# Kernel tuning notes

Hardware: AMD Instinct MI355X
Metric: run time of the kernel (lower is better)

## Reference

```python
import jax, jax.numpy as jnp
import numpy as np

N_NODES = 50000


def gcn_conv(x, edge_index, W, b):
    """PyG GCNConv: h = x @ W; add self-loops; symmetric deg^-1/2 norm; scatter-add; + bias."""
    h = x @ W                                   # [N, C_out]
    n = x.shape[0]
    loops = jnp.arange(n, dtype=edge_index.dtype)
    src = jnp.concatenate([edge_index[0], loops])   # [E + N]
    dst = jnp.concatenate([edge_index[1], loops])   # [E + N]
    deg = jax.ops.segment_sum(jnp.ones_like(src, dtype=h.dtype), dst, num_segments=n)
    dinv = jnp.where(deg > 0, jax.lax.rsqrt(deg), 0.0)
    norm = dinv[src] * dinv[dst]                # [E + N]
    msg = h[src] * norm[:, None]                # gather + edgewise scale
    out = jax.ops.segment_sum(msg, dst, num_segments=n)  # scatter-add
    return out + b


def setup_inputs() -> dict:
    key = jax.random.key(0)
    k1, k2, k3, k4 = jax.random.split(key, 4)
    x = jax.random.normal(k1, (N_NODES, 128), dtype=jnp.float32)
    edge_index = jax.random.randint(k2, (2, 800000), 0, N_NODES, dtype=jnp.int32)
    W1 = jax.random.normal(k3, (128, 128), dtype=jnp.float32) * (1.0 / np.sqrt(128))
    b1 = jnp.zeros((128,), dtype=jnp.float32)
    W2 = jax.random.normal(k4, (128, 64), dtype=jnp.float32) * (1.0 / np.sqrt(128))
    b2 = jnp.zeros((64,), dtype=jnp.float32)
    return {"x": x, "edge_index": edge_index, "W1": W1, "b1": b1, "W2": W2, "b2": b2}


def reference(x, edge_index, W1, b1, W2, b2):
    h = gcn_conv(x, edge_index, W1, b1)
    h = jax.nn.relu(h)
    out = gcn_conv(h, edge_index, W2, b2)
    return out
```

## Files before the change

### kernel.cpp

```cpp
#include <hip/hip_runtime.h>
#include <hip/hip_bf16.h>
#include <math.h>

#define N_NODES 50000
#define N_EDGES 800000
#define NSLICE 8
#define SLICE_NODES 6400
#define CSR_W 48
#define EDGE_CHUNKS ((N_EDGES + 1023) / 1024)

typedef unsigned int uint;
typedef unsigned short ushort;
typedef __attribute__((ext_vector_type(8))) short bf16x8;
typedef __attribute__((ext_vector_type(4))) float f32x4;

__device__ __forceinline__ float bf16_lo(uint u) { return __uint_as_float(u << 16); }
__device__ __forceinline__ float bf16_hi(uint u) { return __uint_as_float(u & 0xFFFF0000u); }
__device__ __forceinline__ ushort f2bf(float a) {
    return __bfloat16_as_ushort(__float2bfloat16(a));
}
__device__ __forceinline__ uint pack_bf2(float a, float b) {
    return ((uint)f2bf(b) << 16) | (uint)f2bf(a);
}

__global__ __launch_bounds__(256) void setup_kernel(const float* __restrict__ W1,
                                                    const float* __restrict__ W2,
                                                    int* __restrict__ counts,
                                                    ushort* __restrict__ W1t,
                                                    ushort* __restrict__ W2t,
                                                    ushort* __restrict__ h1pad,
                                                    ushort* __restrict__ h2pad) {
    int i = blockIdx.x * 256 + threadIdx.x;
    if (i < N_NODES) { counts[i] = 0; return; }
    i -= N_NODES;
    if (i < 128 * 128) {
        int k = i >> 7, n = i & 127;
        W1t[n * 128 + k] = f2bf(W1[i]);
        return;
    }
    i -= 128 * 128;
    if (i < 128 * 64) {
        int k = i >> 6, n = i & 63;
        W2t[n * 128 + k] = f2bf(W2[i]);
        return;
    }
    i -= 128 * 64;
    if (i < 128) { h1pad[i] = 0; return; }
    i -= 128;
    if (i < 64) h2pad[i] = 0;
}

__global__ __launch_bounds__(256) void build_kernel(const int* __restrict__ ei,
                                                    int* __restrict__ counts,
                                                    int* __restrict__ csr) {
    int slice = blockIdx.x & (NSLICE - 1);
    int chunk = blockIdx.x / NSLICE;
    int lo = slice * SLICE_NODES;
    int hi = lo + SLICE_NODES;
    int base = chunk * 1024 + threadIdx.x * 4;
    if (base + 3 < N_EDGES) {
        int4 d = *reinterpret_cast<const int4*>(ei + N_EDGES + base);
        int4 s = *reinterpret_cast<const int4*>(ei + base);
        if (d.x >= lo && d.x < hi) {
            int r = atomicAdd(&counts[d.x], 1);
            if (r < CSR_W) csr[d.x * CSR_W + r] = s.x;
        }
        if (d.y >= lo && d.y < hi) {
            int r = atomicAdd(&counts[d.y], 1);
            if (r < CSR_W) csr[d.y * CSR_W + r] = s.y;
        }
        if (d.z >= lo && d.z < hi) {
            int r = atomicAdd(&counts[d.z], 1);
            if (r < CSR_W) csr[d.z * CSR_W + r] = s.z;
        }
        if (d.w >= lo && d.w < hi) {
            int r = atomicAdd(&counts[d.w], 1);
            if (r < CSR_W) csr[d.w * CSR_W + r] = s.w;
        }
    }
}

template <int C_OUT, bool A_F32>
__global__ __launch_bounds__(256) void gemm_mfma(const void* __restrict__ Ain,
                                                 const ushort* __restrict__ Wt,
                                                 const int* __restrict__ counts,
                                                 ushort* __restrict__ H) {
    int lane = threadIdx.x & 63;
    int w = threadIdx.x >> 6;
    int m = lane & 15;
    int q = lane >> 4;
    int rowTile, nbase;
    if constexpr (C_OUT == 128) {
        rowTile = blockIdx.x * 2 + (w >> 1);
        nbase = (w & 1) * 64;
    } else {
        rowTile = blockIdx.x * 4 + w;
        nbase = 0;
    }
    if (rowTile >= N_NODES / 16) return;

    bf16x8 afrag[4];
    if constexpr (A_F32) {
        const float* arow = (const float*)Ain + (size_t)(rowTile * 16 + m) * 128 + q * 8;
#pragma unroll
        for (int kt = 0; kt < 4; kt++) {
            float4 lo = *reinterpret_cast<const float4*>(arow + kt * 32);
            float4 hi = *reinterpret_cast<const float4*>(arow + kt * 32 + 4);
            uint4 u;
            u.x = pack_bf2(lo.x, lo.y);
            u.y = pack_bf2(lo.z, lo.w);
            u.z = pack_bf2(hi.x, hi.y);
            u.w = pack_bf2(hi.z, hi.w);
            afrag[kt] = *reinterpret_cast<bf16x8*>(&u);
        }
    } else {
        const ushort* arow = (const ushort*)Ain + (size_t)(rowTile * 16 + m) * 128 + q * 8;
#pragma unroll
        for (int kt = 0; kt < 4; kt++)
            afrag[kt] = *reinterpret_cast<const bf16x8*>(arow + kt * 32);
    }

    const ushort* brow = Wt + (size_t)(nbase + m) * 128 + q * 8;
    f32x4 acc[4];
#pragma unroll
    for (int nt = 0; nt < 4; nt++) {
        acc[nt] = {0.f, 0.f, 0.f, 0.f};
        const ushort* bp = brow + (size_t)nt * 16 * 128;
#pragma unroll
        for (int kt = 0; kt < 4; kt++) {
            bf16x8 bfrag = *reinterpret_cast<const bf16x8*>(bp + kt * 32);
            acc[nt] = __builtin_amdgcn_mfma_f32_16x16x32_bf16(afrag[kt], bfrag, acc[nt], 0, 0, 0);
        }
    }

    int rbase = rowTile * 16 + q * 4;
#pragma unroll
    for (int r = 0; r < 4; r++) {
        float dn = rsqrtf((float)(counts[rbase + r] + 1));
#pragma unroll
        for (int nt = 0; nt < 4; nt++) {
            H[(size_t)(rbase + r) * C_OUT + nbase + nt * 16 + m] =
                f2bf(acc[nt][r] * dn);
        }
    }
}

template <int C, bool RELU, bool OUT_BF16>
__global__ __launch_bounds__(256) void agg_kernel(const __hip_bfloat16* __restrict__ Hb,
                                                  const int* __restrict__ counts,
                                                  const int* __restrict__ csr,
                                                  const float* __restrict__ bias,
                                                  void* __restrict__ OUT) {
    int wave = threadIdx.x >> 6;
    int lane = threadIdx.x & 63;
    int n = blockIdx.x * 4 + wave;
    if (n >= N_NODES) return;

    int cntF = counts[n];
    float dn = rsqrtf((float)(cntF + 1));
    int cnt = (cntF < CSR_W) ? cntF : CSR_W;
    int e0 = n * CSR_W;
    int my = (lane < cnt) ? csr[e0 + lane] : N_NODES;

    if constexpr (C == 128) {
        int ql = lane & 15;
        int quarter = lane >> 4;
        float a[8];
        {
            uint4 u = reinterpret_cast<const uint4*>(Hb + (size_t)n * C)[ql];
            a[0] = quarter ? 0.f : bf16_lo(u.x);
            a[1] = quarter ? 0.f : bf16_hi(u.x);
            a[2] = quarter ? 0.f : bf16_lo(u.y);
            a[3] = quarter ? 0.f : bf16_hi(u.y);
            a[4] = quarter ? 0.f : bf16_lo(u.z);
            a[5] = quarter ? 0.f : bf16_hi(u.z);
            a[6] = quarter ? 0.f : bf16_lo(u.w);
            a[7] = quarter ? 0.f : bf16_hi(u.w);
        }
        for (int j = 0; j < cnt; j += 32) {
            int rem = cnt - j;
            int s[8];
            uint4 v[8];
#pragma unroll
            for (int k = 0; k < 8; k++) s[k] = __shfl(my, j + 4 * k + quarter, 64);
#pragma unroll
            for (int k = 0; k < 8; k++) {
                if (4 * k < rem)
                    v[k] = reinterpret_cast<const uint4*>(Hb + (size_t)s[k] * C)[ql];
                else
                    v[k] = make_uint4(0, 0, 0, 0);
            }
#pragma unroll
            for (int k = 0; k < 8; k++) {
                a[0] += bf16_lo(v[k].x);
                a[1] += bf16_hi(v[k].x);
                a[2] += bf16_lo(v[k].y);
                a[3] += bf16_hi(v[k].y);
                a[4] += bf16_lo(v[k].z);
                a[5] += bf16_hi(v[k].z);
                a[6] += bf16_lo(v[k].w);
                a[7] += bf16_hi(v[k].w);
            }
        }
#pragma unroll
        for (int r = 0; r < 8; r++) {
            a[r] += __shfl_xor(a[r], 16, 64);
            a[r] += __shfl_xor(a[r], 32, 64);
        }
        if (quarter == 0) {
            float o[8];
#pragma unroll
            for (int r = 0; r < 8; r++) {
                o[r] = fmaf(a[r], dn, bias[8 * ql + r]);
                if (RELU) o[r] = fmaxf(o[r], 0.f);
            }
            if constexpr (OUT_BF16) {
                uint4 u;
                u.x = pack_bf2(o[0], o[1]);
                u.y = pack_bf2(o[2], o[3]);
                u.z = pack_bf2(o[4], o[5]);
                u.w = pack_bf2(o[6], o[7]);
                reinterpret_cast<uint4*>(OUT)[(size_t)n * 16 + ql] = u;
            } else {
                reinterpret_cast<float4*>(OUT)[(size_t)n * 32 + 2 * ql] =
                    make_float4(o[0], o[1], o[2], o[3]);
                reinterpret_cast<float4*>(OUT)[(size_t)n * 32 + 2 * ql + 1] =
                    make_float4(o[4], o[5], o[6], o[7]);
            }
        }
    } else {
        int gl = lane & 7;
        int group = lane >> 3;
        float a[8];
        {
            uint4 u = reinterpret_cast<const uint4*>(Hb + (size_t)n * C)[gl];
            a[0] = group ? 0.f : bf16_lo(u.x);
            a[1] = group ? 0.f : bf16_hi(u.x);
            a[2] = group ? 0.f : bf16_lo(u.y);
            a[3] = group ? 0.f : bf16_hi(u.y);
            a[4] = group ? 0.f : bf16_lo(u.z);
            a[5] = group ? 0.f : bf16_hi(u.z);
            a[6] = group ? 0.f : bf16_lo(u.w);
            a[7] = group ? 0.f : bf16_hi(u.w);
        }
        {
            int s[8];
            uint4 v[8];
#pragma unroll
            for (int k = 0; k < 8; k++) s[k] = __shfl(my, 8 * k + group, 64);
#pragma unroll
            for (int k = 0; k < 8; k++) {
                if (8 * k < cnt)
                    v[k] = reinterpret_cast<const uint4*>(Hb + (size_t)s[k] * C)[gl];
                else
                    v[k] = make_uint4(0, 0, 0, 0);
            }
#pragma unroll
            for (int k = 0; k < 8; k++) {
                a[0] += bf16_lo(v[k].x);
                a[1] += bf16_hi(v[k].x);
                a[2] += bf16_lo(v[k].y);
                a[3] += bf16_hi(v[k].y);
                a[4] += bf16_lo(v[k].z);
                a[5] += bf16_hi(v[k].z);
                a[6] += bf16_lo(v[k].w);
                a[7] += bf16_hi(v[k].w);
            }
        }
#pragma unroll
        for (int r = 0; r < 8; r++) {
            a[r] += __shfl_xor(a[r], 8, 64);
            a[r] += __shfl_xor(a[r], 16, 64);
            a[r] += __shfl_xor(a[r], 32, 64);
        }
        if (group == 0) {
            float o[8];
#pragma unroll
            for (int r = 0; r < 8; r++) {
                o[r] = fmaf(a[r], dn, bias[8 * gl + r]);
                if (RELU) o[r] = fmaxf(o[r], 0.f);
            }
            if constexpr (OUT_BF16) {
                uint4 u;
                u.x = pack_bf2(o[0], o[1]);
                u.y = pack_bf2(o[2], o[3]);
                u.z = pack_bf2(o[4], o[5]);
                u.w = pack_bf2(o[6], o[7]);
                reinterpret_cast<uint4*>(OUT)[(size_t)n * 8 + gl] = u;
            } else {
                reinterpret_cast<float4*>(OUT)[(size_t)n * 16 + 2 * gl] =
                    make_float4(o[0], o[1], o[2], o[3]);
                reinterpret_cast<float4*>(OUT)[(size_t)n * 16 + 2 * gl + 1] =
                    make_float4(o[4], o[5], o[6], o[7]);
            }
        }
    }
}

extern "C" void kernel_launch(void* const* d_in, const int* in_sizes, int n_in,
                              void* d_out, int out_size, void* d_ws, size_t ws_size,
                              hipStream_t stream) {
    const float* x  = (const float*)d_in[0];
    const int*   ei = (const int*)d_in[1];
    const float* W1 = (const float*)d_in[2];
    const float* b1 = (const float*)d_in[3];
    const float* W2 = (const float*)d_in[4];
    const float* b2 = (const float*)d_in[5];
    float* out = (float*)d_out;

    char* ws = (char*)d_ws;
    auto alloc = [&](size_t bytes) -> char* {
        char* p = ws;
        ws += (bytes + 255) / 256 * 256;
        return p;
    };
    int* counts = (int*)alloc((size_t)N_NODES * 4);
    int* csr = (int*)alloc((size_t)N_NODES * CSR_W * 4);
    ushort* W1t = (ushort*)alloc((size_t)128 * 128 * 2);
    ushort* W2t = (ushort*)alloc((size_t)64 * 128 * 2);
    ushort* h1 = (ushort*)alloc((size_t)(N_NODES + 1) * 128 * 2);
    ushort* g1 = (ushort*)alloc((size_t)N_NODES * 128 * 2);
    ushort* h2 = (ushort*)alloc((size_t)(N_NODES + 1) * 64 * 2);

    const int SETUP_N = N_NODES + 128 * 128 + 128 * 64 + 128 + 64;
    setup_kernel<<<(SETUP_N + 255) / 256, 256, 0, stream>>>(
        W1, W2, counts, W1t, W2t, h1 + (size_t)N_NODES * 128, h2 + (size_t)N_NODES * 64);
    build_kernel<<<EDGE_CHUNKS * NSLICE, 256, 0, stream>>>(ei, counts, csr);

    gemm_mfma<128, true><<<(N_NODES / 16 + 1) / 2, 256, 0, stream>>>(x, W1t, counts, h1);
    agg_kernel<128, true, true><<<(N_NODES + 3) / 4, 256, 0, stream>>>(
        (const __hip_bfloat16*)h1, counts, csr, b1, g1);
    gemm_mfma<64, false><<<(N_NODES / 16 + 3) / 4, 256, 0, stream>>>(g1, W2t, counts, h2);
    agg_kernel<64, false, false><<<(N_NODES + 3) / 4, 256, 0, stream>>>(
        (const __hip_bfloat16*)h2, counts, csr, b2, out);
}
```

Measured before the change: 137.7 us.

## Fuse CSR build with first GEMM and move source-degree scaling into aggregation

```diff
diff --git a/kernel.cpp b/kernel.cpp
--- a/kernel.cpp
+++ b/kernel.cpp
@@ -8,6 +8,8 @@
 #define SLICE_NODES 6400
 #define CSR_W 48
 #define EDGE_CHUNKS ((N_EDGES + 1023) / 1024)
+#define BUILD_BLOCKS (EDGE_CHUNKS * NSLICE)
+#define GEMM1_BLOCKS ((N_NODES / 16 + 1) / 2)
 
 typedef unsigned int uint;
 typedef unsigned short ushort;
@@ -31,8 +33,8 @@
                                                     ushort* __restrict__ h1pad,
                                                     ushort* __restrict__ h2pad) {
     int i = blockIdx.x * 256 + threadIdx.x;
-    if (i < N_NODES) { counts[i] = 0; return; }
-    i -= N_NODES;
+    if (i < N_NODES + 1) { counts[i] = 0; return; }
+    i -= N_NODES + 1;
     if (i < 128 * 128) {
         int k = i >> 7, n = i & 127;
         W1t[n * 128 + k] = f2bf(W1[i]);
@@ -50,77 +52,64 @@
     if (i < 64) h2pad[i] = 0;
 }
 
-__global__ __launch_bounds__(256) void build_kernel(const int* __restrict__ ei,
-                                                    int* __restrict__ counts,
-                                                    int* __restrict__ csr) {
-    int slice = blockIdx.x & (NSLICE - 1);
-    int chunk = blockIdx.x / NSLICE;
-    int lo = slice * SLICE_NODES;
-    int hi = lo + SLICE_NODES;
-    int base = chunk * 1024 + threadIdx.x * 4;
-    if (base + 3 < N_EDGES) {
-        int4 d = *reinterpret_cast<const int4*>(ei + N_EDGES + base);
-        int4 s = *reinterpret_cast<const int4*>(ei + base);
-        if (d.x >= lo && d.x < hi) {
-            int r = atomicAdd(&counts[d.x], 1);
-            if (r < CSR_W) csr[d.x * CSR_W + r] = s.x;
-        }
-        if (d.y >= lo && d.y < hi) {
-            int r = atomicAdd(&counts[d.y], 1);
-            if (r < CSR_W) csr[d.y * CSR_W + r] = s.y;
-        }
-        if (d.z >= lo && d.z < hi) {
-            int r = atomicAdd(&counts[d.z], 1);
-            if (r < CSR_W) csr[d.z * CSR_W + r] = s.z;
-        }
-        if (d.w >= lo && d.w < hi) {
-            int r = atomicAdd(&counts[d.w], 1);
-            if (r < CSR_W) csr[d.w * CSR_W + r] = s.w;
-        }
-    }
-}
-
-template <int C_OUT, bool A_F32>
-__global__ __launch_bounds__(256) void gemm_mfma(const void* __restrict__ Ain,
-                                                 const ushort* __restrict__ Wt,
-                                                 const int* __restrict__ counts,
-                                                 ushort* __restrict__ H) {
+__global__ __launch_bounds__(256) void fused_build_gemm1(const int* __restrict__ ei,
+                                                         int* __restrict__ counts,
+                                                         int* __restrict__ csr,
+                                                         const float* __restrict__ X,
+                                                         const ushort* __restrict__ W1t,
+                                                         ushort* __restrict__ H) {
+    if (blockIdx.x < BUILD_BLOCKS) {
+        int slice = blockIdx.x & (NSLICE - 1);
+        int chunk = blockIdx.x / NSLICE;
+        int lo = slice * SLICE_NODES;
+        int hi = lo + SLICE_NODES;
+        int base = chunk * 1024 + threadIdx.x * 4;
+        if (base + 3 < N_EDGES) {
+            int4 d = *reinterpret_cast<const int4*>(ei + N_EDGES + base);
+            int4 s = *reinterpret_cast<const int4*>(ei + base);
+            if (d.x >= lo && d.x < hi) {
+                int r = atomicAdd(&counts[d.x], 1);
+                if (r < CSR_W) csr[d.x * CSR_W + r] = s.x;
+            }
+            if (d.y >= lo && d.y < hi) {
+                int r = atomicAdd(&counts[d.y], 1);
+                if (r < CSR_W) csr[d.y * CSR_W + r] = s.y;
+            }
+            if (d.z >= lo && d.z < hi) {
+                int r = atomicAdd(&counts[d.z], 1);
+                if (r < CSR_W) csr[d.z * CSR_W + r] = s.z;
+            }
+            if (d.w >= lo && d.w < hi) {
+                int r = atomicAdd(&counts[d.w], 1);
+                if (r < CSR_W) csr[d.w * CSR_W + r] = s.w;
+            }
+        }
+        return;
+    }
+    int bid = blockIdx.x - BUILD_BLOCKS;
     int lane = threadIdx.x & 63;
     int w = threadIdx.x >> 6;
     int m = lane & 15;
     int q = lane >> 4;
-    int rowTile, nbase;
-    if constexpr (C_OUT == 128) {
-        rowTile = blockIdx.x * 2 + (w >> 1);
-        nbase = (w & 1) * 64;
-    } else {
-        rowTile = blockIdx.x * 4 + w;
-        nbase = 0;
-    }
+    int rowTile = bid * 2 + (w >> 1);
+    int nbase = (w & 1) * 64;
     if (rowTile >= N_NODES / 16) return;
 
+    const float* arow = X + (size_t)(rowTile * 16 + m) * 128 + q * 8;
     bf16x8 afrag[4];
-    if constexpr (A_F32) {
-        const float* arow = (const float*)Ain + (size_t)(rowTile * 16 + m) * 128 + q * 8;
-#pragma unroll
-        for (int kt = 0; kt < 4; kt++) {
-            float4 lo = *reinterpret_cast<const float4*>(arow + kt * 32);
-            float4 hi = *reinterpret_cast<const float4*>(arow + kt * 32 + 4);
-            uint4 u;
-            u.x = pack_bf2(lo.x, lo.y);
-            u.y = pack_bf2(lo.z, lo.w);
-            u.z = pack_bf2(hi.x, hi.y);
-            u.w = pack_bf2(hi.z, hi.w);
-            afrag[kt] = *reinterpret_cast<bf16x8*>(&u);
-        }
-    } else {
-        const ushort* arow = (const ushort*)Ain + (size_t)(rowTile * 16 + m) * 128 + q * 8;
-#pragma unroll
-        for (int kt = 0; kt < 4; kt++)
-            afrag[kt] = *reinterpret_cast<const bf16x8*>(arow + kt * 32);
-    }
-
-    const ushort* brow = Wt + (size_t)(nbase + m) * 128 + q * 8;
+#pragma unroll
+    for (int kt = 0; kt < 4; kt++) {
+        float4 lo4 = *reinterpret_cast<const float4*>(arow + kt * 32);
+        float4 hi4 = *reinterpret_cast<const float4*>(arow + kt * 32 + 4);
+        uint4 u;
+        u.x = pack_bf2(lo4.x, lo4.y);
+        u.y = pack_bf2(lo4.z, lo4.w);
+        u.z = pack_bf2(hi4.x, hi4.y);
+        u.w = pack_bf2(hi4.z, hi4.w);
+        afrag[kt] = *reinterpret_cast<bf16x8*>(&u);
+    }
+
+    const ushort* brow = W1t + (size_t)(nbase + m) * 128 + q * 8;
     f32x4 acc[4];
 #pragma unroll
     for (int nt = 0; nt < 4; nt++) {
@@ -136,16 +125,55 @@
     int rbase = rowTile * 16 + q * 4;
 #pragma unroll
     for (int r = 0; r < 4; r++) {
+#pragma unroll
+        for (int nt = 0; nt < 4; nt++) {
+            H[(size_t)(rbase + r) * 128 + nbase + nt * 16 + m] = f2bf(acc[nt][r]);
+        }
+    }
+}
+
+__global__ __launch_bounds__(256) void gemm2_kernel(const ushort* __restrict__ Ain,
+                                                    const ushort* __restrict__ Wt,
+                                                    const int* __restrict__ counts,
+                                                    ushort* __restrict__ H) {
+    int lane = threadIdx.x & 63;
+    int w = threadIdx.x >> 6;
+    int m = lane & 15;
+    int q = lane >> 4;
+    int rowTile = blockIdx.x * 4 + w;
+    if (rowTile >= N_NODES / 16) return;
+
+    const ushort* arow = Ain + (size_t)(rowTile * 16 + m) * 128 + q * 8;
+    bf16x8 afrag[4];
+#pragma unroll
+    for (int kt = 0; kt < 4; kt++)
+        afrag[kt] = *reinterpret_cast<const bf16x8*>(arow + kt * 32);
+
+    const ushort* brow = Wt + (size_t)m * 128 + q * 8;
+    f32x4 acc[4];
+#pragma unroll
+    for (int nt = 0; nt < 4; nt++) {
+        acc[nt] = {0.f, 0.f, 0.f, 0.f};
+        const ushort* bp = brow + (size_t)nt * 16 * 128;
+#pragma unroll
+        for (int kt = 0; kt < 4; kt++) {
+            bf16x8 bfrag = *reinterpret_cast<const bf16x8*>(bp + kt * 32);
+            acc[nt] = __builtin_amdgcn_mfma_f32_16x16x32_bf16(afrag[kt], bfrag, acc[nt], 0, 0, 0);
+        }
+    }
+
+    int rbase = rowTile * 16 + q * 4;
+#pragma unroll
+    for (int r = 0; r < 4; r++) {
         float dn = rsqrtf((float)(counts[rbase + r] + 1));
 #pragma unroll
         for (int nt = 0; nt < 4; nt++) {
-            H[(size_t)(rbase + r) * C_OUT + nbase + nt * 16 + m] =
-                f2bf(acc[nt][r] * dn);
-        }
-    }
-}
-
-template <int C, bool RELU, bool OUT_BF16>
+            H[(size_t)(rbase + r) * 64 + nt * 16 + m] = f2bf(acc[nt][r] * dn);
+        }
+    }
+}
+
+template <int C, bool RELU, bool OUT_BF16, bool SRC_SCALE>
 __global__ __launch_bounds__(256) void agg_kernel(const __hip_bfloat16* __restrict__ Hb,
                                                   const int* __restrict__ counts,
                                                   const int* __restrict__ csr,
@@ -161,6 +189,8 @@
     int cnt = (cntF < CSR_W) ? cntF : CSR_W;
     int e0 = n * CSR_W;
     int my = (lane < cnt) ? csr[e0 + lane] : N_NODES;
+    float mys = 1.f;
+    if constexpr (SRC_SCALE) mys = rsqrtf((float)(counts[my] + 1));
 
     if constexpr (C == 128) {
         int ql = lane & 15;
@@ -168,21 +198,26 @@
         float a[8];
         {
             uint4 u = reinterpret_cast<const uint4*>(Hb + (size_t)n * C)[ql];
-            a[0] = quarter ? 0.f : bf16_lo(u.x);
-            a[1] = quarter ? 0.f : bf16_hi(u.x);
-            a[2] = quarter ? 0.f : bf16_lo(u.y);
-            a[3] = quarter ? 0.f : bf16_hi(u.y);
-            a[4] = quarter ? 0.f : bf16_lo(u.z);
-            a[5] = quarter ? 0.f : bf16_hi(u.z);
-            a[6] = quarter ? 0.f : bf16_lo(u.w);
-            a[7] = quarter ? 0.f : bf16_hi(u.w);
+            float self = SRC_SCALE ? dn : 1.f;
+            a[0] = quarter ? 0.f : self * bf16_lo(u.x);
+            a[1] = quarter ? 0.f : self * bf16_hi(u.x);
+            a[2] = quarter ? 0.f : self * bf16_lo(u.y);
+            a[3] = quarter ? 0.f : self * bf16_hi(u.y);
+            a[4] = quarter ? 0.f : self * bf16_lo(u.z);
+            a[5] = quarter ? 0.f : self * bf16_hi(u.z);
+            a[6] = quarter ? 0.f : self * bf16_lo(u.w);
+            a[7] = quarter ? 0.f : self * bf16_hi(u.w);
         }
         for (int j = 0; j < cnt; j += 32) {
             int rem = cnt - j;
             int s[8];
+            float ds[8];
             uint4 v[8];
 #pragma unroll
-            for (int k = 0; k < 8; k++) s[k] = __shfl(my, j + 4 * k + quarter, 64);
+            for (int k = 0; k < 8; k++) {
+                s[k] = __shfl(my, j + 4 * k + quarter, 64);
+                if (SRC_SCALE) ds[k] = __shfl(mys, j + 4 * k + quarter, 64);
+            }
 #pragma unroll
             for (int k = 0; k < 8; k++) {
                 if (4 * k < rem)
@@ -192,14 +227,15 @@
             }
 #pragma unroll
             for (int k = 0; k < 8; k++) {
-                a[0] += bf16_lo(v[k].x);
-                a[1] += bf16_hi(v[k].x);
-                a[2] += bf16_lo(v[k].y);
-                a[3] += bf16_hi(v[k].y);
-                a[4] += bf16_lo(v[k].z);
-                a[5] += bf16_hi(v[k].z);
-                a[6] += bf16_lo(v[k].w);
-                a[7] += bf16_hi(v[k].w);
+                float w0 = SRC_SCALE ? ds[k] : 1.f;
+                a[0] = fmaf(w0, bf16_lo(v[k].x), a[0]);
+                a[1] = fmaf(w0, bf16_hi(v[k].x), a[1]);
+                a[2] = fmaf(w0, bf16_lo(v[k].y), a[2]);
+                a[3] = fmaf(w0, bf16_hi(v[k].y), a[3]);
+                a[4] = fmaf(w0, bf16_lo(v[k].z), a[4]);
+                a[5] = fmaf(w0, bf16_hi(v[k].z), a[5]);
+                a[6] = fmaf(w0, bf16_lo(v[k].w), a[6]);
+                a[7] = fmaf(w0, bf16_hi(v[k].w), a[7]);
             }
         }
 #pragma unroll
@@ -314,7 +350,7 @@
         ws += (bytes + 255) / 256 * 256;
         return p;
     };
-    int* counts = (int*)alloc((size_t)N_NODES * 4);
+    int* counts = (int*)alloc((size_t)(N_NODES + 1) * 4);
     int* csr = (int*)alloc((size_t)N_NODES * CSR_W * 4);
     ushort* W1t = (ushort*)alloc((size_t)128 * 128 * 2);
     ushort* W2t = (ushort*)alloc((size_t)64 * 128 * 2);
@@ -322,15 +358,14 @@
     ushort* g1 = (ushort*)alloc((size_t)N_NODES * 128 * 2);
     ushort* h2 = (ushort*)alloc((size_t)(N_NODES + 1) * 64 * 2);
 
-    const int SETUP_N = N_NODES + 128 * 128 + 128 * 64 + 128 + 64;
+    const int SETUP_N = (N_NODES + 1) + 128 * 128 + 128 * 64 + 128 + 64;
     setup_kernel<<<(SETUP_N + 255) / 256, 256, 0, stream>>>(
         W1, W2, counts, W1t, W2t, h1 + (size_t)N_NODES * 128, h2 + (size_t)N_NODES * 64);
-    build_kernel<<<EDGE_CHUNKS * NSLICE, 256, 0, stream>>>(ei, counts, csr);
-
-    gemm_mfma<128, true><<<(N_NODES / 16 + 1) / 2, 256, 0, stream>>>(x, W1t, counts, h1);
-    agg_kernel<128, true, true><<<(N_NODES + 3) / 4, 256, 0, stream>>>(
+    fused_build_gemm1<<<BUILD_BLOCKS + GEMM1_BLOCKS, 256, 0, stream>>>(
+        ei, counts, csr, x, W1t, h1);
+    agg_kernel<128, true, true, true><<<(N_NODES + 3) / 4, 256, 0, stream>>>(
         (const __hip_bfloat16*)h1, counts, csr, b1, g1);
-    gemm_mfma<64, false><<<(N_NODES / 16 + 3) / 4, 256, 0, stream>>>(g1, W2t, counts, h2);
-    agg_kernel<64, false, false><<<(N_NODES + 3) / 4, 256, 0, stream>>>(
+    gemm2_kernel<<<(N_NODES / 16 + 3) / 4, 256, 0, stream>>>(g1, W2t, counts, h2);
+    agg_kernel<64, false, false, false><<<(N_NODES + 3) / 4, 256, 0, stream>>>(
         (const __hip_bfloat16*)h2, counts, csr, b2, out);
 }
```

New measurement: 138.0 us. No clear change (+0.2%).
